# Kernel tuning notes

Hardware: AMD Instinct MI355X
Metric: run time of the kernel (lower is better)

The kernel has to match this reference:

```python
import jax, jax.numpy as jnp
import numpy as np

I, J, B, H = 256, 256, 64, 1024
NHID, NCLS = 1024, 3


def setup_inputs() -> dict:
    key = jax.random.key(0)
    ks = jax.random.split(key, 12)
    inp = {
        "P_enc": jax.random.normal(ks[0], (I, B, H), jnp.float32),
        "H_enc": jax.random.normal(ks[1], (J, B, H), jnp.float32),
        "P_emb": jax.random.normal(ks[2], (I, B, H), jnp.float32),
        "H_emb": jax.random.normal(ks[3], (J, B, H), jnp.float32),
        "prem_mask": jax.random.bernoulli(ks[4], 0.15, (I, B)),
        "hypo_mask": jax.random.bernoulli(ks[5], 0.15, (J, B)),
        # compare MLP: Linear(2H, NHID) -> ReLU -> Linear(NHID, NHID) -> ReLU
        "cW1": jax.random.normal(ks[6], (2 * H, NHID), jnp.float32) * 0.02,
        "cb1": jnp.zeros((NHID,), jnp.float32),
        "cW2": jax.random.normal(ks[7], (NHID, NHID), jnp.float32) * 0.02,
        "cb2": jnp.zeros((NHID,), jnp.float32),
        # agg MLP: Linear(2*NHID, NHID) -> ReLU -> Linear(NHID, NCLS)
        "aW1": jax.random.normal(ks[8], (2 * NHID, NHID), jnp.float32) * 0.02,
        "ab1": jnp.zeros((NHID,), jnp.float32),
        "aW2": jax.random.normal(ks[9], (NHID, NCLS), jnp.float32) * 0.02,
        "ab2": jnp.zeros((NCLS,), jnp.float32),
    }
    return inp


def reference(P_enc, H_enc, P_emb, H_emb, prem_mask, hypo_mask,
              cW1, cb1, cW2, cb2, aW1, ab1, aW2, ab2):
    # Dropout is identity at inference.
    def compare(x):
        h = jax.nn.relu(x @ cW1 + cb1)
        return jax.nn.relu(h @ cW2 + cb2)

    # S[b,i,j] = <P_enc[i,b,:], H_enc[j,b,:]>
    S = jnp.einsum('ibh,jbh->bij', P_enc, H_enc)

    # Premise-side masking on rows i, softmax over premise positions (axis=1)
    S_m = jnp.where(prem_mask.T[:, :, None], -jnp.inf, S)  # [b,i,j]
    P_attn = jax.nn.softmax(S_m, axis=1)
    H_ctx = jnp.einsum('bij,ibh->jbh', P_attn, P_emb)      # [j,b,h]
    H_ctx = jnp.where(hypo_mask[:, :, None], 0.0, H_ctx)
    H_comp = compare(jnp.concatenate([H_emb, H_ctx], axis=-1))  # [j,b,nhid]

    # Hypothesis-side: transpose of the UNMASKED scores
    St = jnp.swapaxes(S, 1, 2)                              # [b,j,i]
    St = jnp.where(hypo_mask.T[:, :, None], -jnp.inf, St)
    H_attn = jax.nn.softmax(St, axis=1)
    P_ctx = jnp.einsum('bji,jbh->ibh', H_attn, H_emb)       # [i,b,h]
    P_ctx = jnp.where(prem_mask[:, :, None], 0.0, P_ctx)
    P_comp = compare(jnp.concatenate([P_emb, P_ctx], axis=-1))  # [i,b,nhid]

    pool = jnp.concatenate([H_comp.sum(axis=0), P_comp.sum(axis=0)], axis=-1)  # [b, 2*nhid]
    out = jax.nn.relu(pool @ aW1 + ab1) @ aW2 + ab2          # [b, ncls]
    return out
```

## Files before the change

kernel.cpp:

```cpp
#include <hip/hip_runtime.h>
#include <cstdint>
#include <cstddef>

typedef unsigned short ushort_t;
typedef unsigned char uchar_t;
typedef __attribute__((ext_vector_type(4))) float f4;
typedef __attribute__((ext_vector_type(4))) unsigned int u4;
typedef __attribute__((ext_vector_type(2))) unsigned int u2;

#define DEVI static __device__ __forceinline__

DEVI ushort_t f2bf(float x) {
  union { float f; unsigned int u; } v; v.f = x;
  unsigned int r = v.u + 0x7fffu + ((v.u >> 16) & 1u);
  return (ushort_t)(r >> 16);
}
DEVI float bf2f(ushort_t b) {
  union { unsigned int u; float f; } v; v.u = ((unsigned int)b) << 16;
  return v.f;
}
DEVI unsigned pk2(ushort_t a, ushort_t b) { return (unsigned)a | ((unsigned)b << 16); }

DEVI void mfma16(f4& c, u4 a, u4 b) {
  asm("v_mfma_f32_16x16x32_bf16 %0, %1, %2, %0" : "+v"(c) : "v"(a), "v"(b));
}

constexpr int LDR = 40;

#if defined(__has_builtin)
#if __has_builtin(__builtin_amdgcn_global_load_lds)
#define HAS_GLD 1
#endif
#endif
#ifndef HAS_GLD
#define HAS_GLD 0
#endif

#if HAS_GLD
typedef const __attribute__((address_space(1))) unsigned int* gas1_t;
typedef __attribute__((address_space(3))) unsigned int* las3_t;
DEVI void gld16(const void* g, void* l) {
  __builtin_amdgcn_global_load_lds((gas1_t)g, (las3_t)l, 16, 0, 0);
}
#endif

DEVI void stage_tile(const ushort_t* __restrict__ src, int srcStride, int k0,
                     ushort_t* lT, int t) {
#if HAS_GLD
  int w = t >> 6, lane = t & 63;
#pragma unroll
  for (int c = 0; c < 2; ++c) {
    int row = c * 64 + w * 16 + (lane >> 2);
    const ushort_t* g = src + (size_t)row * srcStride + k0 + (lane & 3) * 8;
    gld16(g, lT + (c * 64 + w * 16) * 32);
  }
#else
  int row = t >> 1, kp = (t & 1) << 4;
  const ushort_t* g = src + (size_t)row * srcStride + k0 + kp;
  *(u4*)(lT + row * 32 + kp) = *(const u4*)g;
  *(u4*)(lT + row * 32 + kp + 8) = *(const u4*)(g + 8);
#endif
}

DEVI void compute16(const ushort_t* lA, const ushort_t* lB, f4 acc[4][4],
                    int wr, int wc, int fr, int fg) {
  u4 af[4], bfv[4];
#pragma unroll
  for (int m = 0; m < 4; ++m) af[m] = *(const u4*)(lA + (wr + m * 16 + fr) * 32 + (fg << 3));
#pragma unroll
  for (int n = 0; n < 4; ++n) bfv[n] = *(const u4*)(lB + (wc + n * 16 + fr) * 32 + (fg << 3));
#pragma unroll
  for (int m = 0; m < 4; ++m)
#pragma unroll
    for (int n = 0; n < 4; ++n) mfma16(acc[m][n], af[m], bfv[n]);
}

__global__ __launch_bounds__(256) void prep_masks_kernel(
    const uchar_t* __restrict__ prem, const uchar_t* __restrict__ hypo,
    uchar_t* __restrict__ premT, uchar_t* __restrict__ hypoT) {
  __shared__ int flagP, flagH;
  int t = threadIdx.x;
  if (t == 0) { flagP = 0; flagH = 0; }
  __syncthreads();
  int locP = 0, locH = 0;
  for (int i = t; i < 16384; i += 256) {
    if (i & 3) { locP |= prem[i]; locH |= hypo[i]; }
  }
  if (locP) atomicOr(&flagP, 1);
  if (locH) atomicOr(&flagH, 1);
  __syncthreads();
  bool p8 = flagP != 0, h8 = flagH != 0;
  for (int i = t; i < 16384; i += 256) {
    int p = i >> 6, b = i & 63;
    premT[b * 256 + p] = p8 ? prem[i] : prem[i * 4];
    hypoT[b * 256 + p] = h8 ? hypo[i] : hypo[i * 4];
  }
}

__global__ __launch_bounds__(256) void transpose_w_kernel(
    const float* __restrict__ Win, ushort_t* __restrict__ Thi,
    ushort_t* __restrict__ Tlo, int N, int K) {
  __shared__ float tl[64][65];
  int k0 = blockIdx.x * 64, n0 = blockIdx.y * 64;
  int t = threadIdx.x;
#pragma unroll
  for (int it = 0; it < 16; ++it) {
    int idx = t + it * 256;
    int k = idx >> 6, n = idx & 63;
    tl[n][k] = Win[(size_t)(k0 + k) * N + n0 + n];
  }
  __syncthreads();
#pragma unroll
  for (int it = 0; it < 16; ++it) {
    int idx = t + it * 256;
    int n = idx >> 6, k = idx & 63;
    float x = tl[n][k];
    ushort_t h = f2bf(x);
    Thi[(size_t)(n0 + n) * K + k0 + k] = h;
    if (Tlo) Tlo[(size_t)(n0 + n) * K + k0 + k] = f2bf(x - bf2f(h));
  }
}

__global__ __launch_bounds__(256) void gemm_s_kernel(
    const float* __restrict__ Penc, const float* __restrict__ Henc,
    float* __restrict__ S) {
  __shared__ ushort_t lAh[64 * LDR], lAl[64 * LDR], lBh[64 * LDR], lBl[64 * LDR];
  const int t = threadIdx.x;
  const int b = blockIdx.z;
  const int i0 = blockIdx.x * 64, j0 = blockIdx.y * 64;
  const int lda = 64 * 1024;
  const float* Ab = Penc + (size_t)i0 * lda + (size_t)b * 1024;
  const float* Bb = Henc + (size_t)j0 * lda + (size_t)b * 1024;
  const int lane = t & 63, wave = t >> 6;
  const int wr = (wave >> 1) << 5, wc = (wave & 1) << 5;
  const int fr = lane & 15, fg = lane >> 4;

  f4 acc[2][2];
#pragma unroll
  for (int m = 0; m < 2; ++m)
#pragma unroll
    for (int n = 0; n < 2; ++n) acc[m][n] = f4{0.f, 0.f, 0.f, 0.f};

  const int row = t >> 2, kp = (t & 3) << 3;
  for (int k0 = 0; k0 < 1024; k0 += 32) {
    {
      const float* p = Ab + (size_t)row * lda + k0 + kp;
      f4 x0 = *(const f4*)p, x1 = *(const f4*)(p + 4);
      ushort_t hh[8], ll[8];
#pragma unroll
      for (int q = 0; q < 4; ++q) {
        ushort_t h0 = f2bf(x0[q]); hh[q] = h0; ll[q] = f2bf(x0[q] - bf2f(h0));
        ushort_t h1 = f2bf(x1[q]); hh[4 + q] = h1; ll[4 + q] = f2bf(x1[q] - bf2f(h1));
      }
      *(u4*)(lAh + row * LDR + kp) = u4{ pk2(hh[0], hh[1]), pk2(hh[2], hh[3]), pk2(hh[4], hh[5]), pk2(hh[6], hh[7]) };
      *(u4*)(lAl + row * LDR + kp) = u4{ pk2(ll[0], ll[1]), pk2(ll[2], ll[3]), pk2(ll[4], ll[5]), pk2(ll[6], ll[7]) };
    }
    {
      const float* p = Bb + (size_t)row * lda + k0 + kp;
      f4 x0 = *(const f4*)p, x1 = *(const f4*)(p + 4);
      ushort_t hh[8], ll[8];
#pragma unroll
      for (int q = 0; q < 4; ++q) {
        ushort_t h0 = f2bf(x0[q]); hh[q] = h0; ll[q] = f2bf(x0[q] - bf2f(h0));
        ushort_t h1 = f2bf(x1[q]); hh[4 + q] = h1; ll[4 + q] = f2bf(x1[q] - bf2f(h1));
      }
      *(u4*)(lBh + row * LDR + kp) = u4{ pk2(hh[0], hh[1]), pk2(hh[2], hh[3]), pk2(hh[4], hh[5]), pk2(hh[6], hh[7]) };
      *(u4*)(lBl + row * LDR + kp) = u4{ pk2(ll[0], ll[1]), pk2(ll[2], ll[3]), pk2(ll[4], ll[5]), pk2(ll[6], ll[7]) };
    }
    __syncthreads();
    u4 ah[2], al[2], bh[2], bl[2];
#pragma unroll
    for (int m = 0; m < 2; ++m) {
      int off = (wr + m * 16 + fr) * LDR + (fg << 3);
      ah[m] = *(const u4*)(lAh + off);
      al[m] = *(const u4*)(lAl + off);
    }
#pragma unroll
    for (int n = 0; n < 2; ++n) {
      int off = (wc + n * 16 + fr) * LDR + (fg << 3);
      bh[n] = *(const u4*)(lBh + off);
      bl[n] = *(const u4*)(lBl + off);
    }
#pragma unroll
    for (int m = 0; m < 2; ++m)
#pragma unroll
      for (int n = 0; n < 2; ++n) {
        mfma16(acc[m][n], ah[m], bh[n]);
        mfma16(acc[m][n], ah[m], bl[n]);
        mfma16(acc[m][n], al[m], bh[n]);
      }
    __syncthreads();
  }

  float* Sb = S + (size_t)b * 65536;
#pragma unroll
  for (int m = 0; m < 2; ++m)
#pragma unroll
    for (int n = 0; n < 2; ++n)
#pragma unroll
      for (int r = 0; r < 4; ++r) {
        int rrow = i0 + wr + m * 16 + fg * 4 + r;
        int col = j0 + wc + n * 16 + fr;
        Sb[(size_t)rrow * 256 + col] = acc[m][n][r];
      }
}

__global__ __launch_bounds__(256) void softmax_rows_kernel(
    const float* __restrict__ S, const uchar_t* __restrict__ hypoT,
    ushort_t* __restrict__ W) {
  int r = blockIdx.x * 4 + (threadIdx.x >> 6);
  int lane = threadIdx.x & 63;
  int b = r >> 8;
  const float* row = S + (size_t)r * 256;
  f4 x = *(const f4*)(row + lane * 4);
  const uchar_t* mp = hypoT + b * 256 + lane * 4;
  float v0 = mp[0] ? -1e30f : x[0];
  float v1 = mp[1] ? -1e30f : x[1];
  float v2 = mp[2] ? -1e30f : x[2];
  float v3 = mp[3] ? -1e30f : x[3];
  float m = fmaxf(fmaxf(v0, v1), fmaxf(v2, v3));
#pragma unroll
  for (int off = 32; off > 0; off >>= 1) m = fmaxf(m, __shfl_xor(m, off));
  float e0 = expf(v0 - m), e1 = expf(v1 - m), e2 = expf(v2 - m), e3 = expf(v3 - m);
  float s = e0 + e1 + e2 + e3;
#pragma unroll
  for (int off = 32; off > 0; off >>= 1) s += __shfl_xor(s, off);
  float rinv = 1.0f / s;
  ushort_t w0 = f2bf(e0 * rinv), w1 = f2bf(e1 * rinv), w2 = f2bf(e2 * rinv), w3 = f2bf(e3 * rinv);
  *(u2*)(W + (size_t)r * 256 + lane * 4) = u2{ pk2(w0, w1), pk2(w2, w3) };
}

__global__ __launch_bounds__(256) void softmax_cols_kernel(
    const float* __restrict__ S, const uchar_t* __restrict__ premT,
    ushort_t* __restrict__ V) {
  __shared__ float tl[32][257];
  __shared__ float pm[8][32], ps[8][32], mfin[32], rs[32];
  int t = threadIdx.x;
  int jl = t & 31, ig = t >> 5;
  int b = blockIdx.y, j0 = blockIdx.x * 32;
  const float* Sb = S + (size_t)b * 65536;
  const uchar_t* pmsk = premT + b * 256;
  for (int i = ig; i < 256; i += 8)
    tl[jl][i] = pmsk[i] ? -1e30f : Sb[(size_t)i * 256 + j0 + jl];
  __syncthreads();
  float m = -3e30f;
#pragma unroll 8
  for (int ii = 0; ii < 32; ++ii) m = fmaxf(m, tl[jl][ig * 32 + ii]);
  float s = 0.f;
#pragma unroll 8
  for (int ii = 0; ii < 32; ++ii) s += expf(tl[jl][ig * 32 + ii] - m);
  pm[ig][jl] = m; ps[ig][jl] = s;
  __syncthreads();
  if (t < 32) {
    float M = pm[0][t];
#pragma unroll
    for (int g = 1; g < 8; ++g) M = fmaxf(M, pm[g][t]);
    float ss = 0.f;
#pragma unroll
    for (int g = 0; g < 8; ++g) ss += ps[g][t] * expf(pm[g][t] - M);
    mfin[t] = M; rs[t] = 1.0f / ss;
  }
  __syncthreads();
  for (int j2 = 0; j2 < 32; ++j2) {
    float val = expf(tl[j2][t] - mfin[j2]) * rs[j2];
    V[((size_t)b * 256 + j0 + j2) * 256 + t] = f2bf(val);
  }
}

__global__ __launch_bounds__(256) void transpose_pos_h_kernel(
    const float* __restrict__ E, ushort_t* __restrict__ T) {
  __shared__ ushort_t tl[64][65];
  int i0 = blockIdx.x * 64, h0 = blockIdx.y * 64, b = blockIdx.z;
  int t = threadIdx.x;
#pragma unroll
  for (int it = 0; it < 16; ++it) {
    int idx = t + it * 256;
    int i = idx >> 6, h = idx & 63;
    tl[h][i] = f2bf(E[((size_t)(i0 + i) * 64 + b) * 1024 + h0 + h]);
  }
  __syncthreads();
#pragma unroll
  for (int it = 0; it < 16; ++it) {
    int idx = t + it * 256;
    int h = idx >> 6, i = idx & 63;
    T[((size_t)b * 1024 + h0 + h) * 256 + i0 + i] = tl[h][i];
  }
}

__global__ __launch_bounds__(256) void cast_half_kernel(
    const float* __restrict__ E, ushort_t* __restrict__ X) {
  size_t idx = (size_t)blockIdx.x * 256 + threadIdx.x;
  size_t r = idx >> 7;
  int h8 = ((int)idx & 127) << 3;
  const f4* p = (const f4*)(E + r * 1024 + h8);
  f4 a = p[0], c = p[1];
  ushort_t hh[8];
#pragma unroll
  for (int q = 0; q < 4; ++q) { hh[q] = f2bf(a[q]); hh[4 + q] = f2bf(c[q]); }
  *(u4*)(X + r * 2048 + h8) =
      u4{ pk2(hh[0], hh[1]), pk2(hh[2], hh[3]), pk2(hh[4], hh[5]), pk2(hh[6], hh[7]) };
}

DEVI void gemm_2ph(const ushort_t* __restrict__ A, int lda,
                   const ushort_t* __restrict__ B, int ldb, int K,
                   ushort_t (*lA)[128 * 32], ushort_t (*lB)[128 * 32],
                   f4 acc[4][4], int t, int wr, int wc, int fr, int fg) {
  stage_tile(A, lda, 0, lA[0], t);
  stage_tile(B, ldb, 0, lB[0], t);
  __syncthreads();
  int nt = K >> 5;
  for (int tt = 0; tt < nt; ++tt) {
    int cur = tt & 1;
    if (tt + 1 < nt) {
      stage_tile(A, lda, (tt + 1) << 5, lA[cur ^ 1], t);
      stage_tile(B, ldb, (tt + 1) << 5, lB[cur ^ 1], t);
    }
    compute16(lA[cur], lB[cur], acc, wr, wc, fr, fg);
    __syncthreads();
  }
}

__global__ __launch_bounds__(256) void gemm_ctx_kernel(
    const ushort_t* __restrict__ Attn, const ushort_t* __restrict__ T,
    const uchar_t* __restrict__ maskT, ushort_t* __restrict__ X) {
  __shared__ ushort_t lA[2][128 * 32], lB[2][128 * 32];
  int t = threadIdx.x;
  int b = blockIdx.z;
  int m0 = blockIdx.x * 128, n0 = blockIdx.y * 128;
  const ushort_t* A = Attn + (size_t)b * 65536 + (size_t)m0 * 256;
  const ushort_t* B = T + (size_t)b * 262144 + (size_t)n0 * 256;
  int lane = t & 63, wave = t >> 6;
  int wr = (wave >> 1) << 6, wc = (wave & 1) << 6;
  int fr = lane & 15, fg = lane >> 4;
  f4 acc[4][4];
#pragma unroll
  for (int m = 0; m < 4; ++m)
#pragma unroll
    for (int n = 0; n < 4; ++n) acc[m][n] = f4{0.f, 0.f, 0.f, 0.f};
  gemm_2ph(A, 256, B, 256, 256, lA, lB, acc, t, wr, wc, fr, fg);
#pragma unroll
  for (int m = 0; m < 4; ++m)
#pragma unroll
    for (int n = 0; n < 4; ++n)
#pragma unroll
      for (int r = 0; r < 4; ++r) {
        int gm = m0 + wr + m * 16 + fg * 4 + r;
        int gn = n0 + wc + n * 16 + fr;
        float v = maskT[b * 256 + gm] ? 0.f : acc[m][n][r];
        X[((size_t)gm * 64 + b) * 2048 + 1024 + gn] = f2bf(v);
      }
}

__global__ __launch_bounds__(256) void gemm_mlp_kernel(
    const ushort_t* __restrict__ A, int lda, const ushort_t* __restrict__ W,
    int ldw, const float* __restrict__ bias, ushort_t* __restrict__ C, int K) {
  __shared__ ushort_t lA[2][128 * 32], lB[2][128 * 32];
  int t = threadIdx.x;
  int m0 = blockIdx.x * 128, n0 = blockIdx.y * 128;
  int lane = t & 63, wave = t >> 6;
  int wr = (wave >> 1) << 6, wc = (wave & 1) << 6;
  int fr = lane & 15, fg = lane >> 4;
  f4 acc[4][4];
#pragma unroll
  for (int m = 0; m < 4; ++m)
#pragma unroll
    for (int n = 0; n < 4; ++n) acc[m][n] = f4{0.f, 0.f, 0.f, 0.f};
  gemm_2ph(A + (size_t)m0 * lda, lda, W + (size_t)n0 * ldw, ldw, K,
           lA, lB, acc, t, wr, wc, fr, fg);
#pragma unroll
  for (int m = 0; m < 4; ++m)
#pragma unroll
    for (int n = 0; n < 4; ++n)
#pragma unroll
      for (int r = 0; r < 4; ++r) {
        int gm = m0 + wr + m * 16 + fg * 4 + r;
        int gn = n0 + wc + n * 16 + fr;
        float v = acc[m][n][r] + bias[gn];
        v = v > 0.f ? v : 0.f;
        C[(size_t)gm * 1024 + gn] = f2bf(v);
      }
}

__global__ __launch_bounds__(256) void pool_partial_kernel(
    const ushort_t* __restrict__ H2, float* __restrict__ partial, int coff) {
  int jc = blockIdx.x, b = blockIdx.y, t = threadIdx.x;
  float a0 = 0.f, a1 = 0.f, a2 = 0.f, a3 = 0.f;
  for (int j = jc * 32; j < jc * 32 + 32; ++j) {
    u2 v = *(const u2*)(H2 + ((size_t)(j * 64 + b)) * 1024 + t * 4);
    a0 += bf2f((ushort_t)(v[0] & 0xffff));
    a1 += bf2f((ushort_t)(v[0] >> 16));
    a2 += bf2f((ushort_t)(v[1] & 0xffff));
    a3 += bf2f((ushort_t)(v[1] >> 16));
  }
  *(f4*)(partial + ((size_t)(jc * 64 + b)) * 2048 + coff + t * 4) = f4{a0, a1, a2, a3};
}

__global__ __launch_bounds__(256) void pool_final_kernel(
    const float* __restrict__ partial, ushort_t* __restrict__ ph,
    ushort_t* __restrict__ pl) {
  int idx = blockIdx.x * 256 + threadIdx.x;
  int b = idx >> 11, k = idx & 2047;
  float s = 0.f;
#pragma unroll
  for (int jc = 0; jc < 8; ++jc) s += partial[((size_t)(jc * 64 + b)) * 2048 + k];
  ushort_t h = f2bf(s);
  ph[idx] = h;
  pl[idx] = f2bf(s - bf2f(h));
}

__global__ __launch_bounds__(256) void gemm_agg1_kernel(
    const ushort_t* __restrict__ Ph, const ushort_t* __restrict__ Pl,
    const ushort_t* __restrict__ Wh, const ushort_t* __restrict__ Wl,
    const float* __restrict__ bias, float* __restrict__ z) {
  __shared__ ushort_t lAh[64 * LDR], lAl[64 * LDR], lBh[128 * LDR], lBl[128 * LDR];
  int t = threadIdx.x;
  int n0 = blockIdx.x * 128;
  int lane = t & 63, wave = t >> 6;
  int wc = wave * 32;
  int fr = lane & 15, fg = lane >> 4;
  f4 acc[4][2];
#pragma unroll
  for (int m = 0; m < 4; ++m)
#pragma unroll
    for (int n = 0; n < 2; ++n) acc[m][n] = f4{0.f, 0.f, 0.f, 0.f};

  for (int k0 = 0; k0 < 2048; k0 += 32) {
    __syncthreads();
    {
      int row = t >> 2, kp = (t & 3) << 3;
      *(u4*)(lAh + row * LDR + kp) = *(const u4*)(Ph + (size_t)row * 2048 + k0 + kp);
      *(u4*)(lAl + row * LDR + kp) = *(const u4*)(Pl + (size_t)row * 2048 + k0 + kp);
    }
#pragma unroll
    for (int c = 0; c < 2; ++c) {
      int ch = t + (c << 8);
      int row = ch >> 2, kp = (ch & 3) << 3;
      *(u4*)(lBh + row * LDR + kp) = *(const u4*)(Wh + (size_t)(n0 + row) * 2048 + k0 + kp);
      *(u4*)(lBl + row * LDR + kp) = *(const u4*)(Wl + (size_t)(n0 + row) * 2048 + k0 + kp);
    }
    __syncthreads();
    u4 ah[4], al[4], bh[2], bl[2];
#pragma unroll
    for (int m = 0; m < 4; ++m) {
      int off = (m * 16 + fr) * LDR + (fg << 3);
      ah[m] = *(const u4*)(lAh + off);
      al[m] = *(const u4*)(lAl + off);
    }
#pragma unroll
    for (int n = 0; n < 2; ++n) {
      int off = (wc + n * 16 + fr) * LDR + (fg << 3);
      bh[n] = *(const u4*)(lBh + off);
      bl[n] = *(const u4*)(lBl + off);
    }
#pragma unroll
    for (int m = 0; m < 4; ++m)
#pragma unroll
      for (int n = 0; n < 2; ++n) {
        mfma16(acc[m][n], ah[m], bh[n]);
        mfma16(acc[m][n], ah[m], bl[n]);
        mfma16(acc[m][n], al[m], bh[n]);
      }
  }
#pragma unroll
  for (int m = 0; m < 4; ++m)
#pragma unroll
    for (int n = 0; n < 2; ++n)
#pragma unroll
      for (int r = 0; r < 4; ++r) {
        int row = m * 16 + fg * 4 + r;
        int col = n0 + wc + n * 16 + fr;
        float v = acc[m][n][r] + bias[col];
        z[row * 1024 + col] = v > 0.f ? v : 0.f;
      }
}

__global__ __launch_bounds__(64) void agg2_kernel(
    const float* __restrict__ z, const float* __restrict__ aW2,
    const float* __restrict__ ab2, float* __restrict__ out) {
  int b = blockIdx.x, lane = threadIdx.x;
  float a0 = 0.f, a1 = 0.f, a2 = 0.f;
  for (int k = lane; k < 1024; k += 64) {
    float zv = z[b * 1024 + k];
    a0 += zv * aW2[k * 3 + 0];
    a1 += zv * aW2[k * 3 + 1];
    a2 += zv * aW2[k * 3 + 2];
  }
#pragma unroll
  for (int off = 32; off > 0; off >>= 1) {
    a0 += __shfl_xor(a0, off);
    a1 += __shfl_xor(a1, off);
    a2 += __shfl_xor(a2, off);
  }
  if (lane == 0) {
    out[b * 3 + 0] = a0 + ab2[0];
    out[b * 3 + 1] = a1 + ab2[1];
    out[b * 3 + 2] = a2 + ab2[2];
  }
}

extern "C" void kernel_launch(void* const* d_in, const int* in_sizes, int n_in,
                              void* d_out, int out_size, void* d_ws, size_t ws_size,
                              hipStream_t stream) {
  const float* P_enc = (const float*)d_in[0];
  const float* H_enc = (const float*)d_in[1];
  const float* P_emb = (const float*)d_in[2];
  const float* H_emb = (const float*)d_in[3];
  const uchar_t* prem = (const uchar_t*)d_in[4];
  const uchar_t* hypo = (const uchar_t*)d_in[5];
  const float* cW1 = (const float*)d_in[6];
  const float* cb1 = (const float*)d_in[7];
  const float* cW2 = (const float*)d_in[8];
  const float* cb2 = (const float*)d_in[9];
  const float* aW1 = (const float*)d_in[10];
  const float* ab1 = (const float*)d_in[11];
  const float* aW2 = (const float*)d_in[12];
  const float* ab2 = (const float*)d_in[13];

  char* w = (char*)d_ws;
  auto alloc = [&](size_t bytes) { char* p = w; w += bytes; return p; };
  float* S        = (float*)alloc(16777216);
  ushort_t* Wsm   = (ushort_t*)alloc(8388608);
  ushort_t* Vsm   = (ushort_t*)alloc(8388608);
  ushort_t* T     = (ushort_t*)alloc(33554432);
  ushort_t* X     = (ushort_t*)alloc(67108864);
  ushort_t* H1    = (ushort_t*)alloc(33554432);
  ushort_t* H2    = (ushort_t*)alloc(33554432);
  ushort_t* cW1T  = (ushort_t*)alloc(4194304);
  ushort_t* cW2T  = (ushort_t*)alloc(2097152);
  ushort_t* aW1Th = (ushort_t*)alloc(4194304);
  ushort_t* aW1Tl = (ushort_t*)alloc(4194304);
  float* partial  = (float*)alloc(4194304);
  ushort_t* poolh = (ushort_t*)alloc(262144);
  ushort_t* pooll = (ushort_t*)alloc(262144);
  float* z        = (float*)alloc(262144);
  uchar_t* premT  = (uchar_t*)alloc(16384);
  uchar_t* hypoT  = (uchar_t*)alloc(16384);

  prep_masks_kernel<<<1, 256, 0, stream>>>(prem, hypo, premT, hypoT);
  transpose_w_kernel<<<dim3(32, 16), 256, 0, stream>>>(cW1, cW1T, (ushort_t*)nullptr, 1024, 2048);
  transpose_w_kernel<<<dim3(16, 16), 256, 0, stream>>>(cW2, cW2T, (ushort_t*)nullptr, 1024, 1024);
  transpose_w_kernel<<<dim3(32, 16), 256, 0, stream>>>(aW1, aW1Th, aW1Tl, 1024, 2048);

  gemm_s_kernel<<<dim3(4, 4, 64), 256, 0, stream>>>(P_enc, H_enc, S);
  softmax_rows_kernel<<<4096, 256, 0, stream>>>(S, hypoT, Wsm);
  softmax_cols_kernel<<<dim3(8, 64), 256, 0, stream>>>(S, premT, Vsm);

  transpose_pos_h_kernel<<<dim3(4, 16, 64), 256, 0, stream>>>(P_emb, T);
  cast_half_kernel<<<8192, 256, 0, stream>>>(H_emb, X);
  gemm_ctx_kernel<<<dim3(2, 8, 64), 256, 0, stream>>>(Vsm, T, hypoT, X);
  gemm_mlp_kernel<<<dim3(128, 8), 256, 0, stream>>>(X, 2048, cW1T, 2048, cb1, H1, 2048);
  gemm_mlp_kernel<<<dim3(128, 8), 256, 0, stream>>>(H1, 1024, cW2T, 1024, cb2, H2, 1024);
  pool_partial_kernel<<<dim3(8, 64), 256, 0, stream>>>(H2, partial, 0);

  transpose_pos_h_kernel<<<dim3(4, 16, 64), 256, 0, stream>>>(H_emb, T);
  cast_half_kernel<<<8192, 256, 0, stream>>>(P_emb, X);
  gemm_ctx_kernel<<<dim3(2, 8, 64), 256, 0, stream>>>(Wsm, T, premT, X);
  gemm_mlp_kernel<<<dim3(128, 8), 256, 0, stream>>>(X, 2048, cW1T, 2048, cb1, H1, 2048);
  gemm_mlp_kernel<<<dim3(128, 8), 256, 0, stream>>>(H1, 1024, cW2T, 1024, cb2, H2, 1024);
  pool_partial_kernel<<<dim3(8, 64), 256, 0, stream>>>(H2, partial, 1024);

  pool_final_kernel<<<512, 256, 0, stream>>>(partial, poolh, pooll);
  gemm_agg1_kernel<<<8, 256, 0, stream>>>(poolh, pooll, aW1Th, aW1Tl, ab1, z);
  agg2_kernel<<<64, 64, 0, stream>>>(z, aW2, ab2, (float*)d_out);
}
```

Measured before the change: 654.4 us.

## Triple-buffer async LDS pipeline for bf16 GEMMs; double-buffer S-score GEMM

Replaces the two-phase double-buffered GEMM helper with a three-stage LDS ring when direct global-to-LDS loads are available. Staging of tile k+2 overlaps compute on tile k, using explicit vmcnt waits and one barrier per iteration. The split-bf16 score GEMM is also double-buffered so the fp32->bf16 hi/lo conversion of the next tile overlaps the MFMAs. The cost is more LDS per block (occupancy risk) and reliance on hand-placed waitcnt ordering, which is fragile.

Result: no change. 662.6 us (+1.3%).

```diff
diff --git a/kernel.cpp b/kernel.cpp
--- a/kernel.cpp
+++ b/kernel.cpp
@@ -75,6 +75,68 @@
     for (int n = 0; n < 4; ++n) mfma16(acc[m][n], af[m], bfv[n]);
 }
 
+#if HAS_GLD
+DEVI void gemm_pipe(const ushort_t* __restrict__ A, int lda,
+                    const ushort_t* __restrict__ B, int ldb, int K,
+                    ushort_t* lab, f4 acc[4][4], int t, int wr, int wc,
+                    int fr, int fg) {
+  ushort_t* a0 = lab;             ushort_t* b0 = lab + 4096;
+  ushort_t* a1 = lab + 2 * 4096;  ushort_t* b1 = lab + 3 * 4096;
+  ushort_t* a2 = lab + 4 * 4096;  ushort_t* b2 = lab + 5 * 4096;
+  const int nt = K >> 5;
+  stage_tile(A, lda, 0, a0, t);
+  stage_tile(B, ldb, 0, b0, t);
+  stage_tile(A, lda, 32, a1, t);
+  stage_tile(B, ldb, 32, b1, t);
+  for (int tt = 0; tt < nt; ++tt) {
+    if (tt + 1 < nt) asm volatile("s_waitcnt vmcnt(4)" ::: "memory");
+    else             asm volatile("s_waitcnt vmcnt(0)" ::: "memory");
+    asm volatile("s_barrier" ::: "memory");
+    if (tt + 2 < nt) {
+      stage_tile(A, lda, (tt + 2) << 5, a2, t);
+      stage_tile(B, ldb, (tt + 2) << 5, b2, t);
+    }
+    u4 af[4], bfv[4];
+#pragma unroll
+    for (int m = 0; m < 4; ++m) af[m] = *(const u4*)(a0 + (wr + m * 16 + fr) * 32 + (fg << 3));
+#pragma unroll
+    for (int n = 0; n < 4; ++n) bfv[n] = *(const u4*)(b0 + (wc + n * 16 + fr) * 32 + (fg << 3));
+    asm volatile("s_waitcnt lgkmcnt(0)" ::: "memory");
+    __builtin_amdgcn_sched_barrier(0);
+#pragma unroll
+    for (int m = 0; m < 4; ++m)
+#pragma unroll
+      for (int n = 0; n < 4; ++n) mfma16(acc[m][n], af[m], bfv[n]);
+    ushort_t* ta = a0; a0 = a1; a1 = a2; a2 = ta;
+    ushort_t* tb = b0; b0 = b1; b1 = b2; b2 = tb;
+  }
+}
+#else
+DEVI void gemm_pipe(const ushort_t* __restrict__ A, int lda,
+                    const ushort_t* __restrict__ B, int ldb, int K,
+                    ushort_t* lab, f4 acc[4][4], int t, int wr, int wc,
+                    int fr, int fg) {
+  ushort_t* a0 = lab;             ushort_t* b0 = lab + 4096;
+  ushort_t* a1 = lab + 2 * 4096;  ushort_t* b1 = lab + 3 * 4096;
+  stage_tile(A, lda, 0, a0, t);
+  stage_tile(B, ldb, 0, b0, t);
+  __syncthreads();
+  const int nt = K >> 5;
+  for (int tt = 0; tt < nt; ++tt) {
+    ushort_t* ca = (tt & 1) ? a1 : a0;
+    ushort_t* cb = (tt & 1) ? b1 : b0;
+    ushort_t* na = (tt & 1) ? a0 : a1;
+    ushort_t* nb = (tt & 1) ? b0 : b1;
+    if (tt + 1 < nt) {
+      stage_tile(A, lda, (tt + 1) << 5, na, t);
+      stage_tile(B, ldb, (tt + 1) << 5, nb, t);
+    }
+    compute16(ca, cb, acc, wr, wc, fr, fg);
+    __syncthreads();
+  }
+}
+#endif
+
 __global__ __launch_bounds__(256) void prep_masks_kernel(
     const uchar_t* __restrict__ prem, const uchar_t* __restrict__ hypo,
     uchar_t* __restrict__ premT, uchar_t* __restrict__ hypoT) {
@@ -124,7 +186,8 @@
 __global__ __launch_bounds__(256) void gemm_s_kernel(
     const float* __restrict__ Penc, const float* __restrict__ Henc,
     float* __restrict__ S) {
-  __shared__ ushort_t lAh[64 * LDR], lAl[64 * LDR], lBh[64 * LDR], lBl[64 * LDR];
+  __shared__ ushort_t lAh[2][64 * LDR], lAl[2][64 * LDR];
+  __shared__ ushort_t lBh[2][64 * LDR], lBl[2][64 * LDR];
   const int t = threadIdx.x;
   const int b = blockIdx.z;
   const int i0 = blockIdx.x * 64, j0 = blockIdx.y * 64;
@@ -134,6 +197,7 @@
   const int lane = t & 63, wave = t >> 6;
   const int wr = (wave >> 1) << 5, wc = (wave & 1) << 5;
   const int fr = lane & 15, fg = lane >> 4;
+  const int row = t >> 2, kp = (t & 3) << 3;
 
   f4 acc[2][2];
 #pragma unroll
@@ -141,8 +205,7 @@
 #pragma unroll
     for (int n = 0; n < 2; ++n) acc[m][n] = f4{0.f, 0.f, 0.f, 0.f};
 
-  const int row = t >> 2, kp = (t & 3) << 3;
-  for (int k0 = 0; k0 < 1024; k0 += 32) {
+  auto stage = [&](int k0, int bi) {
     {
       const float* p = Ab + (size_t)row * lda + k0 + kp;
       f4 x0 = *(const f4*)p, x1 = *(const f4*)(p + 4);
@@ -152,8 +215,8 @@
         ushort_t h0 = f2bf(x0[q]); hh[q] = h0; ll[q] = f2bf(x0[q] - bf2f(h0));
         ushort_t h1 = f2bf(x1[q]); hh[4 + q] = h1; ll[4 + q] = f2bf(x1[q] - bf2f(h1));
       }
-      *(u4*)(lAh + row * LDR + kp) = u4{ pk2(hh[0], hh[1]), pk2(hh[2], hh[3]), pk2(hh[4], hh[5]), pk2(hh[6], hh[7]) };
-      *(u4*)(lAl + row * LDR + kp) = u4{ pk2(ll[0], ll[1]), pk2(ll[2], ll[3]), pk2(ll[4], ll[5]), pk2(ll[6], ll[7]) };
+      *(u4*)(lAh[bi] + row * LDR + kp) = u4{ pk2(hh[0], hh[1]), pk2(hh[2], hh[3]), pk2(hh[4], hh[5]), pk2(hh[6], hh[7]) };
+      *(u4*)(lAl[bi] + row * LDR + kp) = u4{ pk2(ll[0], ll[1]), pk2(ll[2], ll[3]), pk2(ll[4], ll[5]), pk2(ll[6], ll[7]) };
     }
     {
       const float* p = Bb + (size_t)row * lda + k0 + kp;
@@ -164,22 +227,28 @@
         ushort_t h0 = f2bf(x0[q]); hh[q] = h0; ll[q] = f2bf(x0[q] - bf2f(h0));
         ushort_t h1 = f2bf(x1[q]); hh[4 + q] = h1; ll[4 + q] = f2bf(x1[q] - bf2f(h1));
       }
-      *(u4*)(lBh + row * LDR + kp) = u4{ pk2(hh[0], hh[1]), pk2(hh[2], hh[3]), pk2(hh[4], hh[5]), pk2(hh[6], hh[7]) };
-      *(u4*)(lBl + row * LDR + kp) = u4{ pk2(ll[0], ll[1]), pk2(ll[2], ll[3]), pk2(ll[4], ll[5]), pk2(ll[6], ll[7]) };
-    }
-    __syncthreads();
+      *(u4*)(lBh[bi] + row * LDR + kp) = u4{ pk2(hh[0], hh[1]), pk2(hh[2], hh[3]), pk2(hh[4], hh[5]), pk2(hh[6], hh[7]) };
+      *(u4*)(lBl[bi] + row * LDR + kp) = u4{ pk2(ll[0], ll[1]), pk2(ll[2], ll[3]), pk2(ll[4], ll[5]), pk2(ll[6], ll[7]) };
+    }
+  };
+
+  stage(0, 0);
+  __syncthreads();
+  for (int tt = 0; tt < 32; ++tt) {
+    int cur = tt & 1;
+    if (tt + 1 < 32) stage((tt + 1) << 5, cur ^ 1);
     u4 ah[2], al[2], bh[2], bl[2];
 #pragma unroll
     for (int m = 0; m < 2; ++m) {
       int off = (wr + m * 16 + fr) * LDR + (fg << 3);
-      ah[m] = *(const u4*)(lAh + off);
-      al[m] = *(const u4*)(lAl + off);
+      ah[m] = *(const u4*)(lAh[cur] + off);
+      al[m] = *(const u4*)(lAl[cur] + off);
     }
 #pragma unroll
     for (int n = 0; n < 2; ++n) {
       int off = (wc + n * 16 + fr) * LDR + (fg << 3);
-      bh[n] = *(const u4*)(lBh + off);
-      bl[n] = *(const u4*)(lBl + off);
+      bh[n] = *(const u4*)(lBh[cur] + off);
+      bl[n] = *(const u4*)(lBl[cur] + off);
     }
 #pragma unroll
     for (int m = 0; m < 2; ++m)
@@ -301,29 +370,10 @@
       u4{ pk2(hh[0], hh[1]), pk2(hh[2], hh[3]), pk2(hh[4], hh[5]), pk2(hh[6], hh[7]) };
 }
 
-DEVI void gemm_2ph(const ushort_t* __restrict__ A, int lda,
-                   const ushort_t* __restrict__ B, int ldb, int K,
-                   ushort_t (*lA)[128 * 32], ushort_t (*lB)[128 * 32],
-                   f4 acc[4][4], int t, int wr, int wc, int fr, int fg) {
-  stage_tile(A, lda, 0, lA[0], t);
-  stage_tile(B, ldb, 0, lB[0], t);
-  __syncthreads();
-  int nt = K >> 5;
-  for (int tt = 0; tt < nt; ++tt) {
-    int cur = tt & 1;
-    if (tt + 1 < nt) {
-      stage_tile(A, lda, (tt + 1) << 5, lA[cur ^ 1], t);
-      stage_tile(B, ldb, (tt + 1) << 5, lB[cur ^ 1], t);
-    }
-    compute16(lA[cur], lB[cur], acc, wr, wc, fr, fg);
-    __syncthreads();
-  }
-}
-
 __global__ __launch_bounds__(256) void gemm_ctx_kernel(
     const ushort_t* __restrict__ Attn, const ushort_t* __restrict__ T,
     const uchar_t* __restrict__ maskT, ushort_t* __restrict__ X) {
-  __shared__ ushort_t lA[2][128 * 32], lB[2][128 * 32];
+  __shared__ ushort_t lab[6 * 4096];
   int t = threadIdx.x;
   int b = blockIdx.z;
   int m0 = blockIdx.x * 128, n0 = blockIdx.y * 128;
@@ -337,7 +387,7 @@
   for (int m = 0; m < 4; ++m)
 #pragma unroll
     for (int n = 0; n < 4; ++n) acc[m][n] = f4{0.f, 0.f, 0.f, 0.f};
-  gemm_2ph(A, 256, B, 256, 256, lA, lB, acc, t, wr, wc, fr, fg);
+  gemm_pipe(A, 256, B, 256, 256, lab, acc, t, wr, wc, fr, fg);
 #pragma unroll
   for (int m = 0; m < 4; ++m)
 #pragma unroll
@@ -354,7 +404,7 @@
 __global__ __launch_bounds__(256) void gemm_mlp_kernel(
     const ushort_t* __restrict__ A, int lda, const ushort_t* __restrict__ W,
     int ldw, const float* __restrict__ bias, ushort_t* __restrict__ C, int K) {
-  __shared__ ushort_t lA[2][128 * 32], lB[2][128 * 32];
+  __shared__ ushort_t lab[6 * 4096];
   int t = threadIdx.x;
   int m0 = blockIdx.x * 128, n0 = blockIdx.y * 128;
   int lane = t & 63, wave = t >> 6;
@@ -365,8 +415,8 @@
   for (int m = 0; m < 4; ++m)
 #pragma unroll
     for (int n = 0; n < 4; ++n) acc[m][n] = f4{0.f, 0.f, 0.f, 0.f};
-  gemm_2ph(A + (size_t)m0 * lda, lda, W + (size_t)n0 * ldw, ldw, K,
-           lA, lB, acc, t, wr, wc, fr, fg);
+  gemm_pipe(A + (size_t)m0 * lda, lda, W + (size_t)n0 * ldw, ldw, K,
+            lab, acc, t, wr, wc, fr, fg);
 #pragma unroll
   for (int m = 0; m < 4; ++m)
 #pragma unroll
```
